# Performance work log

Measured on AMD Instinct MI355X. Metric: run time of the kernel, lower is better.

The kernel has to match this reference:

```python
import jax, jax.numpy as jnp
import numpy as np

DIM = 1024
HEADS = 16
DIM_HEAD = 64
INNER = HEADS * DIM_HEAD  # 1024
SCALE = DIM_HEAD ** -0.5


def setup_inputs() -> dict:
    key = jax.random.key(0)
    k0, k1, k2 = jax.random.split(key, 3)
    x = jax.random.normal(k0, (4, 2048, DIM), dtype=jnp.float32)
    ln_gamma = jnp.ones((DIM,), dtype=jnp.float32)
    ln_beta = jnp.zeros((DIM,), dtype=jnp.float32)
    w_qkv = jax.random.normal(k1, (DIM, 3 * INNER), dtype=jnp.float32) * (DIM ** -0.5)
    w_out = jax.random.normal(k2, (INNER, DIM), dtype=jnp.float32) * (INNER ** -0.5)
    b_out = jnp.zeros((DIM,), dtype=jnp.float32)
    return {"x": x, "ln_gamma": ln_gamma, "ln_beta": ln_beta,
            "w_qkv": w_qkv, "w_out": w_out, "b_out": b_out}


def reference(x, ln_gamma, ln_beta, w_qkv, w_out, b_out):
    # LayerNorm over last dim (eps matches torch default 1e-5)
    mu = jnp.mean(x, axis=-1, keepdims=True)
    var = jnp.mean(jnp.square(x - mu), axis=-1, keepdims=True)
    xn = (x - mu) * jax.lax.rsqrt(var + 1e-5) * ln_gamma + ln_beta
    # QKV projection (no bias)
    qkv = xn @ w_qkv  # [b, t, 3*inner]
    q, k, v = jnp.split(qkv, 3, axis=-1)
    B, T, _ = x.shape
    def to_heads(t):
        return t.reshape(B, T, HEADS, DIM_HEAD).transpose(0, 2, 1, 3)  # b h t d
    q, k, v = to_heads(q), to_heads(k), to_heads(v)
    dots = jnp.einsum('bhid,bhjd->bhij', q, k) * SCALE
    attn = jax.nn.softmax(dots, axis=-1)
    out = jnp.einsum('bhij,bhjd->bhid', attn, v)
    out = out.transpose(0, 2, 1, 3).reshape(B, T, INNER)
    return out @ w_out + b_out
```

## Files before the change

kernel.cpp:

```cpp
#include <hip/hip_runtime.h>


#define DIMX 1024
#define TSEQ 2048
#define NB 4
#define NH 16
#define DH 64
#define NROWS (NB * TSEQ)
#define QSCALE 0.18033688011112042f

typedef __bf16 bf16_t;
typedef __bf16 bf16x8 __attribute__((ext_vector_type(8)));
typedef __bf16 bf16x4 __attribute__((ext_vector_type(4)));
typedef float f32x4 __attribute__((ext_vector_type(4)));

#if __has_builtin(__builtin_amdgcn_exp2f)
#define EXP2F __builtin_amdgcn_exp2f
#else
#define EXP2F exp2f
#endif

__device__ __forceinline__ bf16x4 cvt4(f32x4 v) {
    return __builtin_convertvector(v, bf16x4);
}
__device__ __forceinline__ void async16(const bf16_t* g, bf16_t* l) {
    __builtin_amdgcn_global_load_lds(
        (const __attribute__((address_space(1))) unsigned int*)g,
        (__attribute__((address_space(3))) unsigned int*)l, 16, 0, 0);
}

__global__ __launch_bounds__(256) void ln_kernel(
    const float* __restrict__ x, const float* __restrict__ g,
    const float* __restrict__ b, bf16_t* __restrict__ xn) {
    int row = blockIdx.x, tid = threadIdx.x;
    const float4 xv = *(const float4*)(x + (size_t)row * DIMX + tid * 4);
    float s = xv.x + xv.y + xv.z + xv.w;
    float q = xv.x * xv.x + xv.y * xv.y + xv.z * xv.z + xv.w * xv.w;
    for (int o = 32; o > 0; o >>= 1) {
        s += __shfl_xor(s, o);
        q += __shfl_xor(q, o);
    }
    __shared__ float2 red[4];
    int wave = tid >> 6, lane = tid & 63;
    if (lane == 0) red[wave] = make_float2(s, q);
    __syncthreads();
    float2 r0 = red[0], r1 = red[1], r2 = red[2], r3 = red[3];
    s = r0.x + r1.x + r2.x + r3.x;
    q = r0.y + r1.y + r2.y + r3.y;
    float mu = s * (1.0f / DIMX);
    float var = q * (1.0f / DIMX) - mu * mu;
    float rstd = rsqrtf(var + 1e-5f);
    float4 gv = *(const float4*)(g + tid * 4);
    float4 bv = *(const float4*)(b + tid * 4);
    f32x4 r;
    r[0] = (xv.x - mu) * rstd * gv.x + bv.x;
    r[1] = (xv.y - mu) * rstd * gv.y + bv.y;
    r[2] = (xv.z - mu) * rstd * gv.z + bv.z;
    r[3] = (xv.w - mu) * rstd * gv.w + bv.w;
    *(bf16x4*)(xn + (size_t)row * DIMX + tid * 4) = cvt4(r);
}

__global__ __launch_bounds__(256) void transpose_cast(
    const float* __restrict__ src, bf16_t* __restrict__ dst, int R, int C) {
    __shared__ float tile[32][33];
    int c0 = blockIdx.x * 32, r0 = blockIdx.y * 32;
    int tx = threadIdx.x, ty = threadIdx.y;
    for (int i = ty; i < 32; i += 8)
        tile[i][tx] = src[(size_t)(r0 + i) * C + c0 + tx];
    __syncthreads();
    for (int i = ty; i < 32; i += 8)
        dst[(size_t)(c0 + i) * R + r0 + tx] = (bf16_t)tile[tx][i];
}

template <int MODE>
__global__ __launch_bounds__(256) void gemm128(
    const bf16_t* __restrict__ A, const bf16_t* __restrict__ BT,
    void* __restrict__ Cout, const float* __restrict__ bias, int M, int N, int K) {
    __shared__ __align__(16) bf16_t As[128 * 32];
    __shared__ __align__(16) bf16_t Bs[128 * 32];
    int tid = threadIdx.x, lane = tid & 63, wave = tid >> 6;
    int lm = lane & 15, quad = lane >> 4;
    int wr = wave >> 1, wc = wave & 1;
    int n0 = blockIdx.x * 128, m0 = blockIdx.y * 128;
    const bf16_t* ga = A + (size_t)(m0 + (tid >> 2)) * K + (tid & 3) * 8;
    const bf16_t* gb = BT + (size_t)(n0 + (tid >> 2)) * K + (tid & 3) * 8;
    bf16_t* la = &As[tid * 8];
    bf16_t* lb = &Bs[tid * 8];
    f32x4 zero = {0.f, 0.f, 0.f, 0.f};
    f32x4 acc[4][4];
#pragma unroll
    for (int i = 0; i < 4; ++i)
#pragma unroll
        for (int j = 0; j < 4; ++j) acc[i][j] = zero;

    for (int k0 = 0; k0 < K; k0 += 32) {
        __syncthreads();
        async16(ga + k0, la);
        async16(ga + (size_t)64 * K + k0, la + 2048);
        async16(gb + k0, lb);
        async16(gb + (size_t)64 * K + k0, lb + 2048);
        __syncthreads();
        bf16x8 af[4], bf[4];
#pragma unroll
        for (int t = 0; t < 4; ++t) {
            af[t] = *(const bf16x8*)&As[(wr * 64 + t * 16 + lm) * 32 + quad * 8];
            bf[t] = *(const bf16x8*)&Bs[(wc * 64 + t * 16 + lm) * 32 + quad * 8];
        }
#pragma unroll
        for (int mt = 0; mt < 4; ++mt)
#pragma unroll
            for (int nt = 0; nt < 4; ++nt)
                acc[mt][nt] = __builtin_amdgcn_mfma_f32_16x16x32_bf16(af[mt], bf[nt], acc[mt][nt], 0, 0, 0);
    }

#pragma unroll
    for (int mt = 0; mt < 4; ++mt) {
#pragma unroll
        for (int nt = 0; nt < 4; ++nt) {
            int m = m0 + wr * 64 + mt * 16 + quad * 4;
            int n = n0 + wc * 64 + nt * 16 + lm;
            if (MODE == 1) {
                int sel = n >> 10, nn = n & 1023, h = nn >> 6, d = nn & 63;
                int b = m >> 11, t = m & 2047;
                if (sel == 2) {
                    *(bf16x4*)((bf16_t*)Cout + (size_t)2 * 8388608 +
                               ((size_t)((b * NH + h) * DH + d)) * TSEQ + t) = cvt4(acc[mt][nt]);
                } else {
                    f32x4 sv = acc[mt][nt] * (sel == 0 ? QSCALE : 1.0f);
                    bf16x4 c4 = cvt4(sv);
#pragma unroll
                    for (int r = 0; r < 4; ++r)
                        ((bf16_t*)Cout)[(size_t)sel * 8388608 +
                                        ((size_t)((b * NH + h) * TSEQ + t + r)) * DH + d] = c4[r];
                }
            } else {
                float bn = bias[n];
#pragma unroll
                for (int r = 0; r < 4; ++r)
                    ((float*)Cout)[(size_t)(m + r) * N + n] = acc[mt][nt][r] + bn;
            }
        }
    }
}

__global__ __launch_bounds__(256, 4) void attn_mfma(
    const bf16_t* __restrict__ qkv, bf16_t* __restrict__ o) {
    int bh = blockIdx.y;
    int qt = blockIdx.x;
    const bf16_t* qb = qkv + (size_t)bh * TSEQ * DH;
    const bf16_t* kb = qkv + (size_t)8388608 + (size_t)bh * TSEQ * DH;
    const bf16_t* vb = qkv + (size_t)16777216 + (size_t)bh * DH * TSEQ;
    int tid = threadIdx.x, wave = tid >> 6, lane = tid & 63;
    int lm = lane & 15, quad = lane >> 4, lx = lm & 7;

    __shared__ __align__(16) bf16_t Ks[64 * 64];
    __shared__ __align__(16) bf16_t Vt[64 * 64];
    __shared__ __align__(16) bf16_t Ps[8 * 1024];

    int roff = tid >> 3;
    int cperm = ((tid & 7) ^ (roff & 7)) * 8;
    const bf16_t* kp0 = kb + (size_t)roff * DH + cperm;
    const bf16_t* kp1 = kb + (size_t)(32 + roff) * DH + cperm;
    const bf16_t* vp0 = vb + (size_t)roff * TSEQ + cperm;
    const bf16_t* vp1 = vb + (size_t)(32 + roff) * TSEQ + cperm;
    bf16_t* lk0 = &Ks[tid * 8];
    bf16_t* lk1 = &Ks[(256 + tid) * 8];
    bf16_t* lv0 = &Vt[tid * 8];
    bf16_t* lv1 = &Vt[(256 + tid) * 8];

    bf16x8 qf[2][2];
#pragma unroll
    for (int u = 0; u < 2; ++u)
#pragma unroll
        for (int ks = 0; ks < 2; ++ks)
            qf[u][ks] = *(const bf16x8*)(qb +
                (size_t)(qt * 128 + wave * 32 + u * 16 + lm) * DH + ks * 32 + quad * 8);

    f32x4 zero = {0.f, 0.f, 0.f, 0.f};
    f32x4 m16 = {-16.f, -16.f, -16.f, -16.f};
    f32x4 acc[2][4];
#pragma unroll
    for (int u = 0; u < 2; ++u)
#pragma unroll
        for (int dt = 0; dt < 4; ++dt) acc[u][dt] = zero;
    f32x4 l4[2] = {zero, zero};

    int fo0 = (quad ^ lx) * 8;
    int fo1 = ((4 + quad) ^ lx) * 8;

    for (int jt = 0; jt < TSEQ / 64; ++jt) {
        __syncthreads();
        async16(kp0, lk0);
        async16(kp1, lk1);
        async16(vp0, lv0);
        async16(vp1, lv1);
        kp0 += 64 * DH; kp1 += 64 * DH; vp0 += 64; vp1 += 64;
        __syncthreads();

        f32x4 s[2][4];
#pragma unroll
        for (int nt = 0; nt < 4; ++nt) {
            bf16x8 kf0 = *(const bf16x8*)&Ks[(nt * 16 + lm) * 64 + fo0];
            bf16x8 kf1 = *(const bf16x8*)&Ks[(nt * 16 + lm) * 64 + fo1];
            s[0][nt] = __builtin_amdgcn_mfma_f32_16x16x32_bf16(kf0, qf[0][0], m16, 0, 0, 0);
            s[0][nt] = __builtin_amdgcn_mfma_f32_16x16x32_bf16(kf1, qf[0][1], s[0][nt], 0, 0, 0);
            s[1][nt] = __builtin_amdgcn_mfma_f32_16x16x32_bf16(kf0, qf[1][0], m16, 0, 0, 0);
            s[1][nt] = __builtin_amdgcn_mfma_f32_16x16x32_bf16(kf1, qf[1][1], s[1][nt], 0, 0, 0);
        }

#pragma unroll
        for (int u = 0; u < 2; ++u) {
            int pb = (wave * 2 + u) * 1024 + lm * 64;
#pragma unroll
            for (int nt = 0; nt < 4; ++nt) {
                f32x4 p;
#pragma unroll
                for (int e = 0; e < 4; ++e) p[e] = EXP2F(s[u][nt][e]);
                l4[u] += p;
                *(bf16x4*)&Ps[pb + ((nt * 2 + (quad >> 1)) ^ lx) * 8 + (quad & 1) * 4] = cvt4(p);
            }
        }

        bf16x8 pf[2][2];
#pragma unroll
        for (int u = 0; u < 2; ++u) {
            pf[u][0] = *(const bf16x8*)&Ps[(wave * 2 + u) * 1024 + lm * 64 + fo0];
            pf[u][1] = *(const bf16x8*)&Ps[(wave * 2 + u) * 1024 + lm * 64 + fo1];
        }
#pragma unroll
        for (int dt = 0; dt < 4; ++dt) {
            bf16x8 vf0 = *(const bf16x8*)&Vt[(dt * 16 + lm) * 64 + fo0];
            bf16x8 vf1 = *(const bf16x8*)&Vt[(dt * 16 + lm) * 64 + fo1];
#pragma unroll
            for (int u = 0; u < 2; ++u) {
                acc[u][dt] = __builtin_amdgcn_mfma_f32_16x16x32_bf16(vf0, pf[u][0], acc[u][dt], 0, 0, 0);
                acc[u][dt] = __builtin_amdgcn_mfma_f32_16x16x32_bf16(vf1, pf[u][1], acc[u][dt], 0, 0, 0);
            }
        }
    }

    int b = bh >> 4, h = bh & 15;
#pragma unroll
    for (int u = 0; u < 2; ++u) {
        float l = (l4[u][0] + l4[u][1]) + (l4[u][2] + l4[u][3]);
        l += __shfl_xor(l, 16);
        l += __shfl_xor(l, 32);
        float rl = 1.0f / l;
        int t = qt * 128 + wave * 32 + u * 16 + lm;
#pragma unroll
        for (int dt = 0; dt < 4; ++dt) {
            f32x4 ov = acc[u][dt] * rl;
            *(bf16x4*)(o + ((size_t)(b * TSEQ + t)) * DIMX + h * DH + dt * 16 + quad * 4) = cvt4(ov);
        }
    }
}

extern "C" void kernel_launch(void* const* d_in, const int* in_sizes, int n_in,
                              void* d_out, int out_size, void* d_ws, size_t ws_size,
                              hipStream_t stream) {
    const float* x = (const float*)d_in[0];
    const float* g = (const float*)d_in[1];
    const float* be = (const float*)d_in[2];
    const float* w_qkv = (const float*)d_in[3];
    const float* w_out = (const float*)d_in[4];
    const float* b_out = (const float*)d_in[5];
    float* out = (float*)d_out;
    char* ws = (char*)d_ws;

    bf16_t* xn = (bf16_t*)(ws);
    bf16_t* wqkvT = (bf16_t*)(ws + 16777216);
    bf16_t* woutT = (bf16_t*)(ws + 23068672);
    bf16_t* qkv = (bf16_t*)(ws + 25165824);
    bf16_t* attno = (bf16_t*)(ws + 75497472);

    ln_kernel<<<NROWS, 256, 0, stream>>>(x, g, be, xn);
    transpose_cast<<<dim3(96, 32), dim3(32, 8), 0, stream>>>(w_qkv, wqkvT, 1024, 3072);
    transpose_cast<<<dim3(32, 32), dim3(32, 8), 0, stream>>>(w_out, woutT, 1024, 1024);
    gemm128<1><<<dim3(24, 64), 256, 0, stream>>>(xn, wqkvT, (void*)qkv, nullptr, NROWS, 3072, 1024);
    attn_mfma<<<dim3(16, 64), 256, 0, stream>>>(qkv, attno);
    gemm128<2><<<dim3(8, 64), 256, 0, stream>>>(attno, woutT, (void*)out, b_out, NROWS, 1024, 1024);
}
```

Before: 296.7 us.

## Double-buffer K/V tiles and shrink per-wave P scratch in attention

Splits the K and V shared tiles into two buffers and prefetches the next tile asynchronously while the current one is computed, dropping one barrier per iteration. Also restructures the score loop to process one query sub-tile at a time, reusing a single per-wave P buffer, which halves P scratch. Total LDS rises, which may limit occupancy, and reusing the P buffer adds a write-after-read dependency within the wave.

```diff
diff --git a/kernel.cpp b/kernel.cpp
--- a/kernel.cpp
+++ b/kernel.cpp
@@ -153,9 +153,9 @@
     int tid = threadIdx.x, wave = tid >> 6, lane = tid & 63;
     int lm = lane & 15, quad = lane >> 4, lx = lm & 7;
 
-    __shared__ __align__(16) bf16_t Ks[64 * 64];
-    __shared__ __align__(16) bf16_t Vt[64 * 64];
-    __shared__ __align__(16) bf16_t Ps[8 * 1024];
+    __shared__ __align__(16) bf16_t Ks[2][64 * 64];
+    __shared__ __align__(16) bf16_t Vt[2][64 * 64];
+    __shared__ __align__(16) bf16_t Ps[4 * 1024];
 
     int roff = tid >> 3;
     int cperm = ((tid & 7) ^ (roff & 7)) * 8;
@@ -163,10 +163,7 @@
     const bf16_t* kp1 = kb + (size_t)(32 + roff) * DH + cperm;
     const bf16_t* vp0 = vb + (size_t)roff * TSEQ + cperm;
     const bf16_t* vp1 = vb + (size_t)(32 + roff) * TSEQ + cperm;
-    bf16_t* lk0 = &Ks[tid * 8];
-    bf16_t* lk1 = &Ks[(256 + tid) * 8];
-    bf16_t* lv0 = &Vt[tid * 8];
-    bf16_t* lv1 = &Vt[(256 + tid) * 8];
+    int l0 = tid * 8, l1 = (256 + tid) * 8;
 
     bf16x8 qf[2][2];
 #pragma unroll
@@ -187,50 +184,57 @@
 
     int fo0 = (quad ^ lx) * 8;
     int fo1 = ((4 + quad) ^ lx) * 8;
+    int pb = wave * 1024 + lm * 64;
+
+    async16(kp0, &Ks[0][l0]);
+    async16(kp1, &Ks[0][l1]);
+    async16(vp0, &Vt[0][l0]);
+    async16(vp1, &Vt[0][l1]);
+    kp0 += 64 * DH; kp1 += 64 * DH; vp0 += 64; vp1 += 64;
 
     for (int jt = 0; jt < TSEQ / 64; ++jt) {
+        int cur = jt & 1;
         __syncthreads();
-        async16(kp0, lk0);
-        async16(kp1, lk1);
-        async16(vp0, lv0);
-        async16(vp1, lv1);
-        kp0 += 64 * DH; kp1 += 64 * DH; vp0 += 64; vp1 += 64;
-        __syncthreads();
-
-        f32x4 s[2][4];
+        if (jt + 1 < TSEQ / 64) {
+            async16(kp0, &Ks[cur ^ 1][l0]);
+            async16(kp1, &Ks[cur ^ 1][l1]);
+            async16(vp0, &Vt[cur ^ 1][l0]);
+            async16(vp1, &Vt[cur ^ 1][l1]);
+            kp0 += 64 * DH; kp1 += 64 * DH; vp0 += 64; vp1 += 64;
+        }
+
+        bf16x8 kf[4][2];
 #pragma unroll
         for (int nt = 0; nt < 4; ++nt) {
-            bf16x8 kf0 = *(const bf16x8*)&Ks[(nt * 16 + lm) * 64 + fo0];
-            bf16x8 kf1 = *(const bf16x8*)&Ks[(nt * 16 + lm) * 64 + fo1];
-            s[0][nt] = __builtin_amdgcn_mfma_f32_16x16x32_bf16(kf0, qf[0][0], m16, 0, 0, 0);
-            s[0][nt] = __builtin_amdgcn_mfma_f32_16x16x32_bf16(kf1, qf[0][1], s[0][nt], 0, 0, 0);
-            s[1][nt] = __builtin_amdgcn_mfma_f32_16x16x32_bf16(kf0, qf[1][0], m16, 0, 0, 0);
-            s[1][nt] = __builtin_amdgcn_mfma_f32_16x16x32_bf16(kf1, qf[1][1], s[1][nt], 0, 0, 0);
-        }
-
+            kf[nt][0] = *(const bf16x8*)&Ks[cur][(nt * 16 + lm) * 64 + fo0];
+            kf[nt][1] = *(const bf16x8*)&Ks[cur][(nt * 16 + lm) * 64 + fo1];
+        }
+
+        bf16x8 pf[2][2];
 #pragma unroll
         for (int u = 0; u < 2; ++u) {
-            int pb = (wave * 2 + u) * 1024 + lm * 64;
+            f32x4 s[4];
+#pragma unroll
+            for (int nt = 0; nt < 4; ++nt) {
+                s[nt] = __builtin_amdgcn_mfma_f32_16x16x32_bf16(kf[nt][0], qf[u][0], m16, 0, 0, 0);
+                s[nt] = __builtin_amdgcn_mfma_f32_16x16x32_bf16(kf[nt][1], qf[u][1], s[nt], 0, 0, 0);
+            }
 #pragma unroll
             for (int nt = 0; nt < 4; ++nt) {
                 f32x4 p;
 #pragma unroll
-                for (int e = 0; e < 4; ++e) p[e] = EXP2F(s[u][nt][e]);
+                for (int e = 0; e < 4; ++e) p[e] = EXP2F(s[nt][e]);
                 l4[u] += p;
                 *(bf16x4*)&Ps[pb + ((nt * 2 + (quad >> 1)) ^ lx) * 8 + (quad & 1) * 4] = cvt4(p);
             }
-        }
-
-        bf16x8 pf[2][2];
-#pragma unroll
-        for (int u = 0; u < 2; ++u) {
-            pf[u][0] = *(const bf16x8*)&Ps[(wave * 2 + u) * 1024 + lm * 64 + fo0];
-            pf[u][1] = *(const bf16x8*)&Ps[(wave * 2 + u) * 1024 + lm * 64 + fo1];
-        }
+            pf[u][0] = *(const bf16x8*)&Ps[pb + fo0];
+            pf[u][1] = *(const bf16x8*)&Ps[pb + fo1];
+        }
+
 #pragma unroll
         for (int dt = 0; dt < 4; ++dt) {
-            bf16x8 vf0 = *(const bf16x8*)&Vt[(dt * 16 + lm) * 64 + fo0];
-            bf16x8 vf1 = *(const bf16x8*)&Vt[(dt * 16 + lm) * 64 + fo1];
+            bf16x8 vf0 = *(const bf16x8*)&Vt[cur][(dt * 16 + lm) * 64 + fo0];
+            bf16x8 vf1 = *(const bf16x8*)&Vt[cur][(dt * 16 + lm) * 64 + fo1];
 #pragma unroll
             for (int u = 0; u < 2; ++u) {
                 acc[u][dt] = __builtin_amdgcn_mfma_f32_16x16x32_bf16(vf0, pf[u][0], acc[u][dt], 0, 0, 0);
```

After: 298.6 us. Within noise of the previous version (+0.7%).
